# Kernel tuning notes

Hardware: AMD Instinct MI355X
Metric: run time of the kernel (lower is better)

Reference implementation:

```python
import jax, jax.numpy as jnp
import numpy as np

H = 128  # hidden size


def setup_inputs() -> dict:
    key = jax.random.key(0)
    ks = jax.random.split(key, 16)
    B, N, L = 32, 64, 256
    s_in = 1.0  # fan-in 1 for layer-0 input weights
    s_h = 1.0 / np.sqrt(H)
    u = lambda k, shape, s: jax.random.uniform(k, shape, jnp.float32, -s, s)
    return {
        "x": jax.random.normal(ks[0], (B, N, L), jnp.float32),
        # LSTM layer 0 (input_size=1), PyTorch gate order i,f,g,o
        "W_ih0": u(ks[1], (4 * H, 1), s_h),
        "W_hh0": u(ks[2], (4 * H, H), s_h),
        "b_ih0": u(ks[3], (4 * H,), s_h),
        "b_hh0": u(ks[4], (4 * H,), s_h),
        # LSTM layer 1 (input_size=H)
        "W_ih1": u(ks[5], (4 * H, H), s_h),
        "W_hh1": u(ks[6], (4 * H, H), s_h),
        "b_ih1": u(ks[7], (4 * H,), s_h),
        "b_hh1": u(ks[8], (4 * H,), s_h),
        # MLP head: Linear(H,H) -> ReLU -> Linear(H,1)
        "W1": u(ks[9], (H, H), s_h),
        "b1": u(ks[10], (H,), s_h),
        "W2": u(ks[11], (1, H), s_h),
        "b2": u(ks[12], (1,), s_h),
        "asset_bias": jnp.zeros((N,), jnp.float32),
    }


def _lstm_cell(x_t, h, c, W_ih, W_hh, b_ih, b_hh):
    g = x_t @ W_ih.T + b_ih + h @ W_hh.T + b_hh  # [BN, 4H]
    i, f, gg, o = jnp.split(g, 4, axis=-1)
    c = jax.nn.sigmoid(f) * c + jax.nn.sigmoid(i) * jnp.tanh(gg)
    h = jax.nn.sigmoid(o) * jnp.tanh(c)
    return h, c


def reference(x, W_ih0, W_hh0, b_ih0, b_hh0, W_ih1, W_hh1, b_ih1, b_hh1,
              W1, b1, W2, b2, asset_bias):
    B, N, L = x.shape
    BN = B * N
    # [L, BN, 1] time-major input (input_size = 1)
    xs = jnp.swapaxes(x.reshape(BN, L), 0, 1)[:, :, None]

    def step(carry, x_t):
        h1, c1, h2, c2 = carry
        h1, c1 = _lstm_cell(x_t, h1, c1, W_ih0, W_hh0, b_ih0, b_hh0)
        h2, c2 = _lstm_cell(h1, h2, c2, W_ih1, W_hh1, b_ih1, b_hh1)
        return (h1, c1, h2, c2), None

    z = jnp.zeros((BN, H), x.dtype)
    (h1, c1, h2, c2), _ = jax.lax.scan(step, (z, z, z, z), xs)
    h_last = h2  # last timestep output of top layer (dropout inactive in eval)
    s = jax.nn.relu(h_last @ W1.T + b1) @ W2.T + b2  # [BN, 1]
    s = s.reshape(B, N) + asset_bias
    return jax.nn.softmax(s, axis=1)
```

## Files before the change

### kernel.cpp

```cpp
#include <hip/hip_runtime.h>

#define H 128
#define L 256
#define SB 8
#define NBLK 256
#define NTHR 512

typedef _Float16 f16x8 __attribute__((ext_vector_type(8)));
typedef float f32x4 __attribute__((ext_vector_type(4)));

#define MFMA(accv, av, bv) accv = __builtin_amdgcn_mfma_f32_16x16x32_f16(av, bv, accv, 0, 0, 0)

__device__ __forceinline__ float fsig(float x) {
  return __builtin_amdgcn_rcpf(1.f + __builtin_amdgcn_exp2f(-1.44269504089f * x));
}
__device__ __forceinline__ float ftanh(float x) {
  return 2.f * __builtin_amdgcn_rcpf(1.f + __builtin_amdgcn_exp2f(-2.88539008178f * x)) - 1.f;
}


__global__ __launch_bounds__(NTHR, 2) void lstm_kernel(
    const float* __restrict__ xg,
    const float* __restrict__ Wih0, const float* __restrict__ Whh0,
    const float* __restrict__ bih0, const float* __restrict__ bhh0,
    const float* __restrict__ Wih1, const float* __restrict__ Whh1,
    const float* __restrict__ bih1, const float* __restrict__ bhh1,
    const float* __restrict__ W1,   const float* __restrict__ b1v,
    const float* __restrict__ W2,   const float* __restrict__ b2v,
    const float* __restrict__ abias,
    float* __restrict__ out_scores)
{
  __shared__ __align__(16) _Float16 Whh1_s[512 * H];
  __shared__ __align__(16) float    x_s[L * SB];
  __shared__ __align__(16) _Float16 h1_s[2][16 * H];
  __shared__ __align__(16) _Float16 h2_s[2][16 * H];

  const int tid  = threadIdx.x;
  const int lane = tid & 63;
  const int w    = tid >> 6;
  const int l15  = lane & 15;
  const int lhi  = lane >> 4;
  const int sb   = blockIdx.x * SB;

  for (int i = tid; i < SB * L; i += NTHR) {
    int s = i >> 8, t = i & 255;
    x_s[t * SB + s] = xg[(sb + s) * L + t];
  }
  for (int i = tid; i < 512 * H; i += NTHR) {
    int r = i >> 7, k = i & 127;
    Whh1_s[(r << 7) + (k ^ ((r & 7) << 3))] = (_Float16)Whh1[i];
  }
  for (int i = tid; i < 16 * H; i += NTHR) {
    h1_s[0][i] = (_Float16)0.f; h1_s[1][i] = (_Float16)0.f;
    h2_s[0][i] = (_Float16)0.f; h2_s[1][i] = (_Float16)0.f;
  }

  f16x8 whh0f[4][4], wih1f[4][4];
  float b0r[4], b1r[4], w0r[4];
  #pragma unroll
  for (int n = 0; n < 4; ++n) {
    const int c = (n << 7) + (w << 4) + l15;
    b0r[n] = bih0[c] + bhh0[c];
    b1r[n] = bih1[c] + bhh1[c];
    w0r[n] = Wih0[c];
    #pragma unroll
    for (int kk = 0; kk < 4; ++kk) {
      const float* p0 = Whh0 + c * H + (kk << 5) + (lhi << 3);
      const float* p1 = Wih1 + c * H + (kk << 5) + (lhi << 3);
      f16x8 f0, f1;
      #pragma unroll
      for (int j = 0; j < 8; ++j) { f0[j] = (_Float16)p0[j]; f1[j] = (_Float16)p1[j]; }
      whh0f[n][kk] = f0; wih1f[n][kk] = f1;
    }
  }

  float c1[2] = {0.f, 0.f}, c2[2] = {0.f, 0.f};
  const int colh  = (w << 4) | l15;
  const int rown0 = lhi << 2;
  const int so0   = lhi << 1;
  const int arow  = l15 << 7;
  const int aswz  = (l15 & 7) << 3;
  int wrow[4];
  #pragma unroll
  for (int n = 0; n < 4; ++n) wrow[n] = ((n << 7) + colh) << 7;

  __syncthreads();

  #pragma unroll 1
  for (int t = 0; t < L; ++t) {
    const int cur = t & 1, prv = cur ^ 1;

    f16x8 a1f[4], a2f[4];
    #pragma unroll
    for (int kk = 0; kk < 4; ++kk) {
      const int kb = (kk << 5) + (lhi << 3);
      a1f[kk] = *(const f16x8*)&h1_s[prv][arow + (kb ^ aswz)];
      a2f[kk] = *(const f16x8*)&h2_s[prv][arow + (kb ^ aswz)];
    }

    f32x4 acc[4];
    #pragma unroll
    for (int n = 0; n < 4; ++n) acc[n] = (f32x4){0.f, 0.f, 0.f, 0.f};
    #pragma unroll
    for (int kk = 0; kk < 4; ++kk) {
      MFMA(acc[0], a1f[kk], whh0f[0][kk]);
      MFMA(acc[1], a1f[kk], whh0f[1][kk]);
      MFMA(acc[2], a1f[kk], whh0f[2][kk]);
      MFMA(acc[3], a1f[kk], whh0f[3][kk]);
    }

    const float2 xv = *(const float2*)&x_s[t * SB + so0];
    float h1n[2];
    #pragma unroll
    for (int r = 0; r < 2; ++r) {
      const float x0 = r ? xv.y : xv.x;
      float ig = fsig (acc[0][r] + x0 * w0r[0] + b0r[0]);
      float fg = fsig (acc[1][r] + x0 * w0r[1] + b0r[1]);
      float gg = ftanh(acc[2][r] + x0 * w0r[2] + b0r[2]);
      float og = fsig (acc[3][r] + x0 * w0r[3] + b0r[3]);
      float c = fg * c1[r] + ig * gg;
      c1[r] = c;
      h1n[r] = og * ftanh(c);
    }
    #pragma unroll
    for (int r = 0; r < 2; ++r) {
      const int row = rown0 + r;
      h1_s[cur][(row << 7) + (colh ^ ((row & 7) << 3))] = (_Float16)h1n[r];
    }
    __syncthreads();

    #pragma unroll
    for (int n = 0; n < 4; ++n) acc[n] = (f32x4){0.f, 0.f, 0.f, 0.f};
    #pragma unroll
    for (int kk = 0; kk < 4; ++kk) {
      const int kb = (kk << 5) + (lhi << 3);
      f16x8 a = *(const f16x8*)&h1_s[cur][arow + (kb ^ aswz)];
      MFMA(acc[0], a, wih1f[0][kk]);
      MFMA(acc[1], a, wih1f[1][kk]);
      MFMA(acc[2], a, wih1f[2][kk]);
      MFMA(acc[3], a, wih1f[3][kk]);
    }
    #pragma unroll
    for (int kk = 0; kk < 4; ++kk) {
      const int kb = (kk << 5) + (lhi << 3);
      #pragma unroll
      for (int n = 0; n < 4; ++n) {
        f16x8 b = *(const f16x8*)&Whh1_s[wrow[n] + (kb ^ aswz)];
        MFMA(acc[n], a2f[kk], b);
      }
    }

    float h2n[2];
    #pragma unroll
    for (int r = 0; r < 2; ++r) {
      float ig = fsig (acc[0][r] + b1r[0]);
      float fg = fsig (acc[1][r] + b1r[1]);
      float gg = ftanh(acc[2][r] + b1r[2]);
      float og = fsig (acc[3][r] + b1r[3]);
      float c = fg * c2[r] + ig * gg;
      c2[r] = c;
      h2n[r] = og * ftanh(c);
    }
    #pragma unroll
    for (int r = 0; r < 2; ++r) {
      const int row = rown0 + r;
      h2_s[cur][(row << 7) + (colh ^ ((row & 7) << 3))] = (_Float16)h2n[r];
    }
    __syncthreads();
  }

  float* W1t = (float*)Whh1_s;
  for (int i = tid; i < H * H; i += NTHR) {
    int j = i >> 7, k = i & 127;
    W1t[(k << 7) + j] = W1[i];
  }
  __syncthreads();
  {
    const int s   = w;
    const int row = ((s >> 1) << 2) | (s & 1);
    float a0 = 0.f, a1 = 0.f;
    for (int k = 0; k < H; ++k) {
      float hv = (float)h2_s[1][(row << 7) + (k ^ ((row & 7) << 3))];
      a0 += hv * W1t[(k << 7) + lane];
      a1 += hv * W1t[(k << 7) + lane + 64];
    }
    a0 = fmaxf(a0 + b1v[lane], 0.f);
    a1 = fmaxf(a1 + b1v[lane + 64], 0.f);
    float part = a0 * W2[lane] + a1 * W2[lane + 64];
    #pragma unroll
    for (int off = 32; off >= 1; off >>= 1) part += __shfl_xor(part, off, 64);
    if (lane == 0)
      out_scores[sb + s] = part + b2v[0] + abias[(sb + s) & 63];
  }
}

__global__ void softmax_kernel(float* __restrict__ out) {
  const int b = blockIdx.x, n = threadIdx.x;
  float v = out[(b << 6) + n];
  float m = v;
  #pragma unroll
  for (int off = 32; off >= 1; off >>= 1) m = fmaxf(m, __shfl_xor(m, off, 64));
  float e = __builtin_amdgcn_exp2f((v - m) * 1.44269504089f);
  float s = e;
  #pragma unroll
  for (int off = 32; off >= 1; off >>= 1) s += __shfl_xor(s, off, 64);
  out[(b << 6) + n] = e / s;
}

extern "C" void kernel_launch(void* const* d_in, const int* in_sizes, int n_in,
                              void* d_out, int out_size, void* d_ws, size_t ws_size,
                              hipStream_t stream) {
  (void)in_sizes; (void)n_in; (void)d_ws; (void)ws_size; (void)out_size;
  const float* xg   = (const float*)d_in[0];
  const float* Wih0 = (const float*)d_in[1];
  const float* Whh0 = (const float*)d_in[2];
  const float* bih0 = (const float*)d_in[3];
  const float* bhh0 = (const float*)d_in[4];
  const float* Wih1 = (const float*)d_in[5];
  const float* Whh1 = (const float*)d_in[6];
  const float* bih1 = (const float*)d_in[7];
  const float* bhh1 = (const float*)d_in[8];
  const float* W1   = (const float*)d_in[9];
  const float* b1   = (const float*)d_in[10];
  const float* W2   = (const float*)d_in[11];
  const float* b2   = (const float*)d_in[12];
  const float* ab   = (const float*)d_in[13];
  float* out = (float*)d_out;

  lstm_kernel<<<NBLK, NTHR, 0, stream>>>(xg, Wih0, Whh0, bih0, bhh0,
                                         Wih1, Whh1, bih1, bhh1,
                                         W1, b1, W2, b2, ab, out);
  softmax_kernel<<<32, 64, 0, stream>>>(out);
}
```

Before: 506.6 us.

## Skew layer-1 LSTM one timestep behind layer-0 to merge both into one phase

The time loop is restructured as a wavefront: in iteration t, layer 0 computes step t while layer 1 computes step t-1 using the h1 published in the previous iteration. Both layers' MFMAs read the same h1 fragments and run as one independent batch. Gate math for both layers follows, with one barrier per iteration instead of two. The loop runs L+1 iterations with guarded prologue and epilogue, and needs a second accumulator set, which raises register pressure.

```diff
diff --git a/kernel.cpp b/kernel.cpp
--- a/kernel.cpp
+++ b/kernel.cpp
@@ -87,58 +87,35 @@
   __syncthreads();
 
   #pragma unroll 1
-  for (int t = 0; t < L; ++t) {
-    const int cur = t & 1, prv = cur ^ 1;
+  for (int t = 0; t <= L; ++t) {
+    const int pw = t & 1;
+    const int pr = pw ^ 1;
 
     f16x8 a1f[4], a2f[4];
     #pragma unroll
     for (int kk = 0; kk < 4; ++kk) {
       const int kb = (kk << 5) + (lhi << 3);
-      a1f[kk] = *(const f16x8*)&h1_s[prv][arow + (kb ^ aswz)];
-      a2f[kk] = *(const f16x8*)&h2_s[prv][arow + (kb ^ aswz)];
-    }
-
-    f32x4 acc[4];
-    #pragma unroll
-    for (int n = 0; n < 4; ++n) acc[n] = (f32x4){0.f, 0.f, 0.f, 0.f};
-    #pragma unroll
-    for (int kk = 0; kk < 4; ++kk) {
-      MFMA(acc[0], a1f[kk], whh0f[0][kk]);
-      MFMA(acc[1], a1f[kk], whh0f[1][kk]);
-      MFMA(acc[2], a1f[kk], whh0f[2][kk]);
-      MFMA(acc[3], a1f[kk], whh0f[3][kk]);
-    }
-
-    const float2 xv = *(const float2*)&x_s[t * SB + so0];
-    float h1n[2];
-    #pragma unroll
-    for (int r = 0; r < 2; ++r) {
-      const float x0 = r ? xv.y : xv.x;
-      float ig = fsig (acc[0][r] + x0 * w0r[0] + b0r[0]);
-      float fg = fsig (acc[1][r] + x0 * w0r[1] + b0r[1]);
-      float gg = ftanh(acc[2][r] + x0 * w0r[2] + b0r[2]);
-      float og = fsig (acc[3][r] + x0 * w0r[3] + b0r[3]);
-      float c = fg * c1[r] + ig * gg;
-      c1[r] = c;
-      h1n[r] = og * ftanh(c);
-    }
-    #pragma unroll
-    for (int r = 0; r < 2; ++r) {
-      const int row = rown0 + r;
-      h1_s[cur][(row << 7) + (colh ^ ((row & 7) << 3))] = (_Float16)h1n[r];
-    }
-    __syncthreads();
-
-    #pragma unroll
-    for (int n = 0; n < 4; ++n) acc[n] = (f32x4){0.f, 0.f, 0.f, 0.f};
-    #pragma unroll
-    for (int kk = 0; kk < 4; ++kk) {
-      const int kb = (kk << 5) + (lhi << 3);
-      f16x8 a = *(const f16x8*)&h1_s[cur][arow + (kb ^ aswz)];
-      MFMA(acc[0], a, wih1f[0][kk]);
-      MFMA(acc[1], a, wih1f[1][kk]);
-      MFMA(acc[2], a, wih1f[2][kk]);
-      MFMA(acc[3], a, wih1f[3][kk]);
+      a1f[kk] = *(const f16x8*)&h1_s[pr][arow + (kb ^ aswz)];
+      a2f[kk] = *(const f16x8*)&h2_s[pw][arow + (kb ^ aswz)];
+    }
+
+    f32x4 acc0[4], acc1[4];
+    #pragma unroll
+    for (int n = 0; n < 4; ++n) {
+      acc0[n] = (f32x4){0.f, 0.f, 0.f, 0.f};
+      acc1[n] = (f32x4){0.f, 0.f, 0.f, 0.f};
+    }
+
+    #pragma unroll
+    for (int kk = 0; kk < 4; ++kk) {
+      MFMA(acc0[0], a1f[kk], whh0f[0][kk]);
+      MFMA(acc0[1], a1f[kk], whh0f[1][kk]);
+      MFMA(acc0[2], a1f[kk], whh0f[2][kk]);
+      MFMA(acc0[3], a1f[kk], whh0f[3][kk]);
+      MFMA(acc1[0], a1f[kk], wih1f[0][kk]);
+      MFMA(acc1[1], a1f[kk], wih1f[1][kk]);
+      MFMA(acc1[2], a1f[kk], wih1f[2][kk]);
+      MFMA(acc1[3], a1f[kk], wih1f[3][kk]);
     }
     #pragma unroll
     for (int kk = 0; kk < 4; ++kk) {
@@ -146,25 +123,47 @@
       #pragma unroll
       for (int n = 0; n < 4; ++n) {
         f16x8 b = *(const f16x8*)&Whh1_s[wrow[n] + (kb ^ aswz)];
-        MFMA(acc[n], a2f[kk], b);
-      }
-    }
-
-    float h2n[2];
-    #pragma unroll
-    for (int r = 0; r < 2; ++r) {
-      float ig = fsig (acc[0][r] + b1r[0]);
-      float fg = fsig (acc[1][r] + b1r[1]);
-      float gg = ftanh(acc[2][r] + b1r[2]);
-      float og = fsig (acc[3][r] + b1r[3]);
-      float c = fg * c2[r] + ig * gg;
-      c2[r] = c;
-      h2n[r] = og * ftanh(c);
-    }
-    #pragma unroll
-    for (int r = 0; r < 2; ++r) {
-      const int row = rown0 + r;
-      h2_s[cur][(row << 7) + (colh ^ ((row & 7) << 3))] = (_Float16)h2n[r];
+        MFMA(acc1[n], a2f[kk], b);
+      }
+    }
+
+    if (t < L) {
+      const float2 xv = *(const float2*)&x_s[t * SB + so0];
+      float h1n[2];
+      #pragma unroll
+      for (int r = 0; r < 2; ++r) {
+        const float x0 = r ? xv.y : xv.x;
+        float ig = fsig (acc0[0][r] + x0 * w0r[0] + b0r[0]);
+        float fg = fsig (acc0[1][r] + x0 * w0r[1] + b0r[1]);
+        float gg = ftanh(acc0[2][r] + x0 * w0r[2] + b0r[2]);
+        float og = fsig (acc0[3][r] + x0 * w0r[3] + b0r[3]);
+        float c = fg * c1[r] + ig * gg;
+        c1[r] = c;
+        h1n[r] = og * ftanh(c);
+      }
+      #pragma unroll
+      for (int r = 0; r < 2; ++r) {
+        const int row = rown0 + r;
+        h1_s[pw][(row << 7) + (colh ^ ((row & 7) << 3))] = (_Float16)h1n[r];
+      }
+    }
+    if (t > 0) {
+      float h2n[2];
+      #pragma unroll
+      for (int r = 0; r < 2; ++r) {
+        float ig = fsig (acc1[0][r] + b1r[0]);
+        float fg = fsig (acc1[1][r] + b1r[1]);
+        float gg = ftanh(acc1[2][r] + b1r[2]);
+        float og = fsig (acc1[3][r] + b1r[3]);
+        float c = fg * c2[r] + ig * gg;
+        c2[r] = c;
+        h2n[r] = og * ftanh(c);
+      }
+      #pragma unroll
+      for (int r = 0; r < 2; ++r) {
+        const int row = rown0 + r;
+        h2_s[pr][(row << 7) + (colh ^ ((row & 7) << 3))] = (_Float16)h2n[r];
+      }
     }
     __syncthreads();
   }
```

Result: faster. 474.8 us (-6.3%).
